# Kernel optimization log

Hardware: AMD Instinct MI355X
Metric: run time of the kernel (lower is better)

## Reference

```python
import jax, jax.numpy as jnp
import numpy as np

N = 50000   # nodes
E = 800000  # edges
H = 128     # hidden_dim
K = 4       # Chebyshev order
EPS_BN = 1e-5
EPS_L2 = 1e-12


def setup_inputs() -> dict:
    key = jax.random.key(0)
    ks = jax.random.split(key, 8)
    x = jax.random.normal(ks[0], (N, 3), dtype=jnp.float32)
    edge_index = jax.random.randint(ks[1], (2, E), 0, N, dtype=jnp.int32)

    def lin(k, fi, fo):
        s = 1.0 / np.sqrt(fi)
        return jax.random.uniform(k, (fi, fo), jnp.float32, -s, s)

    def cheb_params(k, fi, fo):
        kk = jax.random.split(k, K)
        W = jnp.stack([lin(kk[i], fi, fo) for i in range(K)])  # [K, fi, fo]
        b = jnp.zeros((fo,), jnp.float32)
        return W, b

    W1, b1 = cheb_params(ks[2], 3, H)
    W2, b2 = cheb_params(ks[3], H, H)
    W3, b3 = cheb_params(ks[4], H, H)
    W4, b4 = cheb_params(ks[5], H, H)
    Wr = lin(ks[6], H, 3)
    br = jnp.zeros((3,), jnp.float32)
    ones = jnp.ones((H,), jnp.float32)
    zeros = jnp.zeros((H,), jnp.float32)
    return {
        'x': x, 'edge_index': edge_index,
        'W1': W1, 'b1': b1, 'W2': W2, 'b2': b2,
        'W3': W3, 'b3': b3, 'W4': W4, 'b4': b4,
        'g1': ones, 'be1': zeros, 'g2': ones, 'be2': zeros,
        'g3': ones, 'be3': zeros, 'Wr': Wr, 'br': br,
    }


def _prop(h, src, dst, norm):
    # one sparse Laplacian application: out[dst] += norm * h[src]
    return jax.ops.segment_sum(norm[:, None] * h[src], dst, num_segments=N)


def _cheb(h, src, dst, norm, W, b):
    # PyG ChebConv with sym normalization, lambda_max=2 -> L_hat edge weights
    # are -D^-1/2 A D^-1/2 with zero diagonal (encoded in norm).
    out = h @ W[0]
    Tx0, Tx1 = h, _prop(h, src, dst, norm)
    out = out + Tx1 @ W[1]
    for k in range(2, W.shape[0]):
        Tx2 = 2.0 * _prop(Tx1, src, dst, norm) - Tx0
        out = out + Tx2 @ W[k]
        Tx0, Tx1 = Tx1, Tx2
    return out + b


def _bn(h, g, b):
    # BatchNorm1d in training mode: batch stats over node dim, biased var
    m = h.mean(axis=0)
    v = h.var(axis=0)
    return g * (h - m) * jax.lax.rsqrt(v + EPS_BN) + b


def reference(x, edge_index, W1, b1, W2, b2, W3, b3, W4, b4,
              g1, be1, g2, be2, g3, be3, Wr, br):
    src, dst = edge_index[0], edge_index[1]
    deg = jax.ops.segment_sum(jnp.ones((E,), jnp.float32), src, num_segments=N)
    dinv = jnp.where(deg > 0, jax.lax.rsqrt(jnp.maximum(deg, 1.0)), 0.0)
    norm = -dinv[src] * dinv[dst]

    h = _bn(jax.nn.leaky_relu(_cheb(x, src, dst, norm, W1, b1)), g1, be1)
    h = _bn(jax.nn.leaky_relu(_cheb(h, src, dst, norm, W2, b2)), g2, be2)
    h = _bn(jax.nn.relu(_cheb(h, src, dst, norm, W3, b3)), g3, be3)
    h = _cheb(h, src, dst, norm, W4, b4)
    # F.normalize(p=2, dim=1)
    h = h / jnp.maximum(jnp.linalg.norm(h, axis=1, keepdims=True), EPS_L2)
    return h @ Wr + br
```

## Files before the change

kernel.cpp:

```cpp
#include <hip/hip_runtime.h>
#include <hip/hip_fp16.h>

#define HD 128

typedef __attribute__((ext_vector_type(8))) _Float16 f16x8;
typedef __attribute__((ext_vector_type(4))) float f32x4;
typedef unsigned int u32;

struct h4s { __half2 a, b; };

__device__ __forceinline__ float lrelu(float x, float s) { return x > 0.f ? x : s * x; }

__global__ void k_edge_count(const int* __restrict__ src, const int* __restrict__ dst,
                             int* __restrict__ degc, int* __restrict__ cnt,
                             int* __restrict__ ledge, int E) {
  int e = blockIdx.x * blockDim.x + threadIdx.x;
  if (e < E) {
    atomicAdd(&degc[src[e]], 1);
    ledge[e] = atomicAdd(&cnt[dst[e]], 1);
  }
}

__global__ __launch_bounds__(1024) void k_scan1(const int* __restrict__ cnt,
                                                int* __restrict__ rowptr,
                                                int* __restrict__ bsums, int n) {
  __shared__ int buf[1024];
  int i = blockIdx.x * 1024 + threadIdx.x;
  int v = (i < n) ? cnt[i] : 0;
  buf[threadIdx.x] = v;
  __syncthreads();
  for (int o = 1; o < 1024; o <<= 1) {
    int t = (threadIdx.x >= (unsigned)o) ? buf[threadIdx.x - o] : 0;
    __syncthreads();
    buf[threadIdx.x] += t;
    __syncthreads();
  }
  if (i < n) rowptr[i] = buf[threadIdx.x] - v;
  if (threadIdx.x == 1023) bsums[blockIdx.x] = buf[1023];
}

__global__ __launch_bounds__(1024) void k_scan3(int* __restrict__ rowptr,
                                                const int* __restrict__ bsums,
                                                const int* __restrict__ degc,
                                                float* __restrict__ dinv, int n, int Etot,
                                                int nb) {
  __shared__ int blockoff;
  if (nb <= 64) {
    if (threadIdx.x < 64) {
      int lane = threadIdx.x;
      int v = (lane < nb) ? bsums[lane] : 0;
      int inc = v;
#pragma unroll
      for (int o = 1; o < 64; o <<= 1) {
        int t = __shfl_up(inc, o, 64);
        if (lane >= o) inc += t;
      }
      if (lane == (int)blockIdx.x) blockoff = inc - v;
    }
  } else if (threadIdx.x == 0) {
    int sum = 0;
    for (int t = 0; t < (int)blockIdx.x; ++t) sum += bsums[t];
    blockoff = sum;
  }
  __syncthreads();
  int i = blockIdx.x * 1024 + threadIdx.x;
  if (i < n) {
    rowptr[i] += blockoff;
    int dg = degc[i];
    dinv[i] = dg > 0 ? rsqrtf((float)dg) : 0.f;
  }
  if (i == 0) rowptr[n] = Etot;
}

__global__ void k_fill(const int* __restrict__ src, const int* __restrict__ dst,
                       const int* __restrict__ ledge, const int* __restrict__ rowptr,
                       const float* __restrict__ dinv, uint2* __restrict__ cw, int E) {
  int e = blockIdx.x * blockDim.x + threadIdx.x;
  if (e < E) {
    int s = src[e], d = dst[e];
    int p = rowptr[d] + ledge[e];
    cw[p] = make_uint2((u32)s, __float_as_uint(-dinv[s] * dinv[d]));
  }
}

__global__ void k_prop3(const int* __restrict__ rowptr, const uint2* __restrict__ cw,
                        const float* __restrict__ Hs, const float* __restrict__ Sub,
                        float* __restrict__ Out, float scale, int n) {
  int r = blockIdx.x * blockDim.x + threadIdx.x;
  if (r >= n) return;
  int b = rowptr[r], e = rowptr[r + 1];
  float a0 = 0.f, a1 = 0.f, a2 = 0.f;
  for (int j = b; j < e; ++j) {
    uint2 m = cw[j];
    int s = (int)m.x;
    float w = __uint_as_float(m.y);
    a0 = fmaf(w, Hs[s * 3 + 0], a0);
    a1 = fmaf(w, Hs[s * 3 + 1], a1);
    a2 = fmaf(w, Hs[s * 3 + 2], a2);
  }
  float r0 = scale * a0, r1 = scale * a1, r2 = scale * a2;
  if (Sub) { r0 -= Sub[r * 3 + 0]; r1 -= Sub[r * 3 + 1]; r2 -= Sub[r * 3 + 2]; }
  Out[r * 3 + 0] = r0; Out[r * 3 + 1] = r1; Out[r * 3 + 2] = r2;
}

template <int PHI>
__global__ __launch_bounds__(256) void k_prop128(
    const int* __restrict__ rowptr, const uint2* __restrict__ cw,
    const __half* __restrict__ Ph, const __half* __restrict__ Sub,
    __half* __restrict__ Outh, float scale, int n,
    const float* __restrict__ gsc, const float* __restrict__ gsh,
    const float* __restrict__ ssc, const float* __restrict__ ssh, float slope) {
  int r = blockIdx.x * 4 + (int)(threadIdx.x >> 6);
  int lane = threadIdx.x & 63;
  if (r >= n) return;
  int b = rowptr[r], e = rowptr[r + 1];
  int fl = (lane & 31) << 2;
  int half = lane >> 5;
  float ax = 0.f, ay = 0.f, az = 0.f, aw = 0.f, ws = 0.f;
  int j = b;
  for (; j + 7 < e; j += 8) {
    h4s h[4];
    float w[4];
#pragma unroll
    for (int q = 0; q < 4; ++q) {
      int idx = j + 2 * q + half;
      uint2 m = cw[idx];
      w[q] = __uint_as_float(m.y);
      h[q] = *(const h4s*)&Ph[(size_t)m.x * HD + fl];
    }
#pragma unroll
    for (int q = 0; q < 4; ++q) {
      float2 f0 = __half22float2(h[q].a);
      float2 f1 = __half22float2(h[q].b);
      if (PHI) {
        f0.x = lrelu(f0.x, slope); f0.y = lrelu(f0.y, slope);
        f1.x = lrelu(f1.x, slope); f1.y = lrelu(f1.y, slope);
        ws += w[q];
      }
      ax = fmaf(w[q], f0.x, ax);
      ay = fmaf(w[q], f0.y, ay);
      az = fmaf(w[q], f1.x, az);
      aw = fmaf(w[q], f1.y, aw);
    }
  }
  for (; j + 1 < e; j += 2) {
    int idx = j + half;
    uint2 m = cw[idx];
    float w = __uint_as_float(m.y);
    h4s h = *(const h4s*)&Ph[(size_t)m.x * HD + fl];
    float2 f0 = __half22float2(h.a);
    float2 f1 = __half22float2(h.b);
    if (PHI) {
      f0.x = lrelu(f0.x, slope); f0.y = lrelu(f0.y, slope);
      f1.x = lrelu(f1.x, slope); f1.y = lrelu(f1.y, slope);
      ws += w;
    }
    ax = fmaf(w, f0.x, ax);
    ay = fmaf(w, f0.y, ay);
    az = fmaf(w, f1.x, az);
    aw = fmaf(w, f1.y, aw);
  }
  if (j < e && half == 0) {
    uint2 m = cw[j];
    float w = __uint_as_float(m.y);
    h4s h = *(const h4s*)&Ph[(size_t)m.x * HD + fl];
    float2 f0 = __half22float2(h.a);
    float2 f1 = __half22float2(h.b);
    if (PHI) {
      f0.x = lrelu(f0.x, slope); f0.y = lrelu(f0.y, slope);
      f1.x = lrelu(f1.x, slope); f1.y = lrelu(f1.y, slope);
      ws += w;
    }
    ax = fmaf(w, f0.x, ax);
    ay = fmaf(w, f0.y, ay);
    az = fmaf(w, f1.x, az);
    aw = fmaf(w, f1.y, aw);
  }
  ax += __shfl_xor(ax, 32, 64);
  ay += __shfl_xor(ay, 32, 64);
  az += __shfl_xor(az, 32, 64);
  aw += __shfl_xor(aw, 32, 64);
  if (PHI) {
    ws += __shfl_xor(ws, 32, 64);
    float4 g4 = *(const float4*)&gsc[fl];
    float4 s4 = *(const float4*)&gsh[fl];
    ax = fmaf(ax, g4.x, ws * s4.x);
    ay = fmaf(ay, g4.y, ws * s4.y);
    az = fmaf(az, g4.z, ws * s4.z);
    aw = fmaf(aw, g4.w, ws * s4.w);
  }
  float4 o = make_float4(scale * ax, scale * ay, scale * az, scale * aw);
  if (Sub) {
    h4s sh4 = *(const h4s*)&Sub[(size_t)r * HD + fl];
    float2 s0 = __half22float2(sh4.a);
    float2 s1 = __half22float2(sh4.b);
    if (ssc != nullptr) {
      float4 c4 = *(const float4*)&ssc[fl];
      float4 d4 = *(const float4*)&ssh[fl];
      s0.x = fmaf(lrelu(s0.x, slope), c4.x, d4.x);
      s0.y = fmaf(lrelu(s0.y, slope), c4.y, d4.y);
      s1.x = fmaf(lrelu(s1.x, slope), c4.z, d4.z);
      s1.y = fmaf(lrelu(s1.y, slope), c4.w, d4.w);
    }
    o.x -= s0.x; o.y -= s0.y; o.z -= s1.x; o.w -= s1.y;
  }
  if (half == 0) {
    h4s ho;
    ho.a = __float22half2_rn(make_float2(o.x, o.y));
    ho.b = __float22half2_rn(make_float2(o.z, o.w));
    *(h4s*)&Outh[(size_t)r * HD + fl] = ho;
  }
}

__global__ __launch_bounds__(128) void k_l1gemm(
    const float* __restrict__ X, const float* __restrict__ T1, const float* __restrict__ T2,
    const float* __restrict__ T3, const float* __restrict__ W1, const float* __restrict__ b1,
    __half* __restrict__ Outh, float* __restrict__ bnsum, float* __restrict__ bnsq,
    float slope, int n, int rpb) {
  int j = threadIdx.x;
  float w[12];
#pragma unroll
  for (int t = 0; t < 4; ++t)
#pragma unroll
    for (int c = 0; c < 3; ++c) w[t * 3 + c] = W1[(t * 3 + c) * HD + j];
  float bj = b1[j];
  int r0 = blockIdx.x * rpb, r1 = min(r0 + rpb, n);
  float s = 0.f, q = 0.f;
  for (int r = r0; r < r1; ++r) {
    float acc = bj;
#pragma unroll
    for (int c = 0; c < 3; ++c) {
      acc = fmaf(X [r * 3 + c], w[0 + c], acc);
      acc = fmaf(T1[r * 3 + c], w[3 + c], acc);
      acc = fmaf(T2[r * 3 + c], w[6 + c], acc);
      acc = fmaf(T3[r * 3 + c], w[9 + c], acc);
    }
    Outh[(size_t)r * HD + j] = __float2half(acc);
    float a = lrelu(acc, slope);
    s += a;
    q = fmaf(a, a, q);
  }
  atomicAdd(&bnsum[j], s);
  atomicAdd(&bnsq[j], q);
}

__global__ void k_wsplit3(const float* __restrict__ W2, const float* __restrict__ W3,
                          const float* __restrict__ W4, uint4* __restrict__ Whi,
                          uint4* __restrict__ Wlo) {
  int flat = blockIdx.x * 256 + threadIdx.x;
  int wsel = flat >> 13;
  int f = flat & 8191;
  const float* W = (wsel == 0) ? W2 : (wsel == 1) ? W3 : W4;
  int n = f & 127, K8 = f >> 7;
  int chunk = K8 >> 2, g = K8 & 3;
  f16x8 hv, lv;
#pragma unroll
  for (int i = 0; i < 8; ++i) {
    int k = chunk * 32 + ((i >> 2) << 4) + g * 4 + (i & 3);
    float v = W[(size_t)k * HD + n];
    _Float16 hh = (_Float16)v;
    _Float16 hl = (_Float16)(v - (float)hh);
    hv[i] = hh;
    lv[i] = hl;
  }
  int slot = chunk * 512 + (n >> 4) * 64 + g * 16 + (n & 15);
  Whi[wsel * 8192 + slot] = *(uint4*)&hv;
  Wlo[wsel * 8192 + slot] = *(uint4*)&lv;
}

__global__ __launch_bounds__(256) void k_gemm4m(
    const __half* __restrict__ T0, const __half* __restrict__ T1,
    const __half* __restrict__ T2, const __half* __restrict__ T3,
    const uint4* __restrict__ Whi, const uint4* __restrict__ Wlo,
    const float* __restrict__ bias, __half* __restrict__ OUTh,
    float* bnsum, float* bnsq, float stat_slope,
    const float* __restrict__ gsc, const float* __restrict__ gsh, float phi_slope,
    int nrows) {
  __shared__ __half sA[2048];
  __shared__ __half sWh[4096], sWl[4096];
  __shared__ float redS[128], redQ[128];

  int tid = threadIdx.x;
  int lane = tid & 63, w = tid >> 6, wr = w >> 1, wc = w & 1;
  int g = (tid >> 4) & 3;
  int ri = tid & 15;
  int row0 = blockIdx.x * 64;
  int arow = row0 + w * 16 + ri;
  bool aval = arow < nrows;

  f32x4 zero = {0.f, 0.f, 0.f, 0.f};
  f32x4 acc[2][4];
#pragma unroll
  for (int mi = 0; mi < 2; ++mi)
#pragma unroll
    for (int nj = 0; nj < 4; ++nj) acc[mi][nj] = zero;

  if (tid < 128) { redS[tid] = 0.f; redQ[tid] = 0.f; }

  for (int chunk = 0; chunk < 16; ++chunk) {
    const __half* Ts = (chunk < 4) ? T0 : (chunk < 8) ? T1 : (chunk < 12) ? T2 : T3;
    int kc = chunk & 3;
    h4s va, vb;
    *(uint2*)&va = make_uint2(0u, 0u);
    *(uint2*)&vb = make_uint2(0u, 0u);
    if (aval) {
      const __half* ap = Ts + (size_t)arow * HD + kc * 32 + g * 4;
      va = *(const h4s*)ap;
      vb = *(const h4s*)(ap + 16);
    }
    size_t wbase = (size_t)chunk * 512;
    uint4 wh0 = Whi[wbase + tid], wh1 = Whi[wbase + 256 + tid];
    uint4 wl0 = Wlo[wbase + tid], wl1 = Wlo[wbase + 256 + tid];

    __syncthreads();

    if (gsc != nullptr && chunk < 4) {
      float fv[8];
      float2 f0 = __half22float2(va.a), f1 = __half22float2(va.b);
      float2 f2 = __half22float2(vb.a), f3 = __half22float2(vb.b);
      fv[0] = f0.x; fv[1] = f0.y; fv[2] = f1.x; fv[3] = f1.y;
      fv[4] = f2.x; fv[5] = f2.y; fv[6] = f3.x; fv[7] = f3.y;
#pragma unroll
      for (int i = 0; i < 8; ++i) {
        int f = kc * 32 + g * 4 + (i & 3) + ((i >> 2) << 4);
        fv[i] = fmaf(lrelu(fv[i], phi_slope), gsc[f], gsh[f]);
      }
      va.a = __float22half2_rn(make_float2(fv[0], fv[1]));
      va.b = __float22half2_rn(make_float2(fv[2], fv[3]));
      vb.a = __float22half2_rn(make_float2(fv[4], fv[5]));
      vb.b = __float22half2_rn(make_float2(fv[6], fv[7]));
    }
    *(h4s*)&sA[tid * 8] = va;
    *(h4s*)&sA[tid * 8 + 4] = vb;
    *(uint4*)&sWh[tid * 8] = wh0;
    *(uint4*)&sWh[(256 + tid) * 8] = wh1;
    *(uint4*)&sWl[tid * 8] = wl0;
    *(uint4*)&sWl[(256 + tid) * 8] = wl1;
    __syncthreads();

    f16x8 a[2], bh[4], bl[4];
#pragma unroll
    for (int mi = 0; mi < 2; ++mi)
      a[mi] = *(const f16x8*)&sA[((wr * 2 + mi) * 64 + lane) * 8];
#pragma unroll
    for (int nj = 0; nj < 4; ++nj) {
      bh[nj] = *(const f16x8*)&sWh[((wc * 4 + nj) * 64 + lane) * 8];
      bl[nj] = *(const f16x8*)&sWl[((wc * 4 + nj) * 64 + lane) * 8];
    }
#pragma unroll
    for (int mi = 0; mi < 2; ++mi)
#pragma unroll
      for (int nj = 0; nj < 4; ++nj) {
        acc[mi][nj] = __builtin_amdgcn_mfma_f32_16x16x32_f16(a[mi], bh[nj], acc[mi][nj], 0, 0, 0);
        acc[mi][nj] = __builtin_amdgcn_mfma_f32_16x16x32_f16(a[mi], bl[nj], acc[mi][nj], 0, 0, 0);
      }
  }

  int l4 = (lane >> 4) * 4, ni = lane & 15;
  bool stats = (bnsum != nullptr);
#pragma unroll
  for (int nj = 0; nj < 4; ++nj) {
    int c = wc * 64 + nj * 16 + ni;
    float bcol = bias[c];
    float s = 0.f, q = 0.f;
#pragma unroll
    for (int mi = 0; mi < 2; ++mi)
#pragma unroll
      for (int j = 0; j < 4; ++j) {
        int row = row0 + (wr * 2 + mi) * 16 + l4 + j;
        if (row < nrows) {
          float v = acc[mi][nj][j] + bcol;
          OUTh[(size_t)row * HD + c] = __float2half(v);
          if (stats) {
            float a = lrelu(v, stat_slope);
            s += a;
            q = fmaf(a, a, q);
          }
        }
      }
    if (stats) {
      s += __shfl_xor(s, 16, 64);
      s += __shfl_xor(s, 32, 64);
      q += __shfl_xor(q, 16, 64);
      q += __shfl_xor(q, 32, 64);
      if (lane < 16) {
        atomicAdd(&redS[c], s);
        atomicAdd(&redQ[c], q);
      }
    }
  }
  if (stats) {
    __syncthreads();
    if (tid < 128) {
      atomicAdd(&bnsum[tid], redS[tid]);
      atomicAdd(&bnsq[tid], redQ[tid]);
    }
  }
}

__global__ void k_bnfin(const float* __restrict__ bsum, const float* __restrict__ bsq,
                        const float* __restrict__ g, const float* __restrict__ be,
                        float* __restrict__ scaleb, float* __restrict__ shiftb, int n) {
  int f = threadIdx.x;
  if (f < HD) {
    float m = bsum[f] / (float)n;
    float v = bsq[f] / (float)n - m * m;
    float rs = rsqrtf(v + 1e-5f);
    float sc = g[f] * rs;
    scaleb[f] = sc;
    shiftb[f] = be[f] - m * sc;
  }
}

__global__ __launch_bounds__(256) void k_final(const __half* __restrict__ Hb,
                                               const float* __restrict__ Wr,
                                               const float* __restrict__ br,
                                               float* __restrict__ out, int n) {
  int r = blockIdx.x * 4 + (int)(threadIdx.x >> 6);
  int lane = threadIdx.x & 63;
  if (r >= n) return;
  float h0 = __half2float(Hb[(size_t)r * HD + lane]);
  float h1 = __half2float(Hb[(size_t)r * HD + 64 + lane]);
  float ss = h0 * h0 + h1 * h1;
#pragma unroll
  for (int o = 32; o; o >>= 1) ss += __shfl_xor(ss, o, 64);
  float inv = 1.f / fmaxf(sqrtf(ss), 1e-12f);
  h0 *= inv; h1 *= inv;
  float o0 = h0 * Wr[lane * 3 + 0] + h1 * Wr[(64 + lane) * 3 + 0];
  float o1 = h0 * Wr[lane * 3 + 1] + h1 * Wr[(64 + lane) * 3 + 1];
  float o2 = h0 * Wr[lane * 3 + 2] + h1 * Wr[(64 + lane) * 3 + 2];
#pragma unroll
  for (int o = 32; o; o >>= 1) {
    o0 += __shfl_xor(o0, o, 64);
    o1 += __shfl_xor(o1, o, 64);
    o2 += __shfl_xor(o2, o, 64);
  }
  if (lane == 0) {
    out[r * 3 + 0] = o0 + br[0];
    out[r * 3 + 1] = o1 + br[1];
    out[r * 3 + 2] = o2 + br[2];
  }
}

extern "C" void kernel_launch(void* const* d_in, const int* in_sizes, int n_in,
                              void* d_out, int out_size, void* d_ws, size_t ws_size,
                              hipStream_t stream) {
  const float* x  = (const float*)d_in[0];
  const int*   ei = (const int*)d_in[1];
  const float* W1 = (const float*)d_in[2];
  const float* b1 = (const float*)d_in[3];
  const float* W2 = (const float*)d_in[4];
  const float* b2 = (const float*)d_in[5];
  const float* W3 = (const float*)d_in[6];
  const float* b3 = (const float*)d_in[7];
  const float* W4 = (const float*)d_in[8];
  const float* b4 = (const float*)d_in[9];
  const float* g1 = (const float*)d_in[10];
  const float* be1= (const float*)d_in[11];
  const float* g2 = (const float*)d_in[12];
  const float* be2= (const float*)d_in[13];
  const float* g3 = (const float*)d_in[14];
  const float* be3= (const float*)d_in[15];
  const float* Wr = (const float*)d_in[16];
  const float* br = (const float*)d_in[17];

  const int N = in_sizes[0] / 3;
  const int E = in_sizes[1] / 2;
  const int* src = ei;
  const int* dst = ei + E;
  float* out = (float*)d_out;

  char* wp = (char*)d_ws;
  size_t used = 0;
  auto alloc = [&](size_t bytes) -> void* {
    void* p = (void*)(wp + used);
    used += (bytes + 255) & ~(size_t)255;
    return p;
  };
  int*   deg2   = (int*)alloc((size_t)2 * N * 4);
  int*   rowptr = (int*)alloc((size_t)(N + 1) * 4);
  float* dinv   = (float*)alloc((size_t)N * 4);
  int*   bsums  = (int*)alloc(256 * 4);
  int*   ledge  = (int*)alloc((size_t)E * 4);
  uint2* cw     = (uint2*)alloc((size_t)E * 8);
  float* t1     = (float*)alloc((size_t)N * 3 * 4);
  float* t2     = (float*)alloc((size_t)N * 3 * 4);
  float* t3     = (float*)alloc((size_t)N * 3 * 4);
  __half* phA   = (__half*)alloc((size_t)N * HD * 2);
  __half* phB   = (__half*)alloc((size_t)N * HD * 2);
  __half* phC   = (__half*)alloc((size_t)N * HD * 2);
  __half* phD   = (__half*)alloc((size_t)N * HD * 2);
  float* stats  = (float*)alloc(6 * HD * 4);
  float* scsh   = (float*)alloc(6 * HD * 4);
  uint4* Whi3   = (uint4*)alloc(3 * 8192 * 16);
  uint4* Wlo3   = (uint4*)alloc(3 * 8192 * 16);
  if (used > ws_size) return;

  int* degc = deg2;
  int* cnt  = deg2 + N;
  float* bnsum1 = stats + 0 * HD; float* bnsq1 = stats + 1 * HD;
  float* bnsum2 = stats + 2 * HD; float* bnsq2 = stats + 3 * HD;
  float* bnsum3 = stats + 4 * HD; float* bnsq3 = stats + 5 * HD;
  float* sc1 = scsh + 0 * HD; float* sh1 = scsh + 1 * HD;
  float* sc2 = scsh + 2 * HD; float* sh2 = scsh + 3 * HD;
  float* sc3 = scsh + 4 * HD; float* sh3 = scsh + 5 * HD;

  const int eb = (E + 255) / 256;
  const int nb = (N + 255) / 256;
  const int pb = (N + 3) / 4;
  const int sb = (N + 1023) / 1024;
  const int gbm = (N + 63) / 64;

  hipMemsetAsync(stats, 0, 6 * HD * 4, stream);
  hipMemsetAsync(deg2, 0, (size_t)2 * N * 4, stream);
  k_edge_count<<<eb, 256, 0, stream>>>(src, dst, degc, cnt, ledge, E);
  k_scan1<<<sb, 1024, 0, stream>>>(cnt, rowptr, bsums, N);
  k_scan3<<<sb, 1024, 0, stream>>>(rowptr, bsums, degc, dinv, N, E, sb);
  k_fill<<<eb, 256, 0, stream>>>(src, dst, ledge, rowptr, dinv, cw, E);
  k_wsplit3<<<96, 256, 0, stream>>>(W2, W3, W4, Whi3, Wlo3);

  k_prop3<<<nb, 256, 0, stream>>>(rowptr, cw, x, nullptr, t1, 1.f, N);
  k_prop3<<<nb, 256, 0, stream>>>(rowptr, cw, t1, x, t2, 2.f, N);
  k_prop3<<<nb, 256, 0, stream>>>(rowptr, cw, t2, t1, t3, 2.f, N);
  k_l1gemm<<<(N + 255) / 256, 128, 0, stream>>>(x, t1, t2, t3, W1, b1, phA,
                                                bnsum1, bnsq1, 0.01f, N, 256);
  k_bnfin<<<1, 128, 0, stream>>>(bnsum1, bnsq1, g1, be1, sc1, sh1, N);

  auto cheb_layer = [&](const uint4* Whi, const uint4* Wlo, const float* bk,
                        const float* psc, const float* psh, float phi_slope,
                        float* bs, float* bq, float stat_slope) {
    k_prop128<1><<<pb, 256, 0, stream>>>(rowptr, cw, phA, nullptr, phB, 1.f, N,
                                         psc, psh, nullptr, nullptr, phi_slope);
    k_prop128<0><<<pb, 256, 0, stream>>>(rowptr, cw, phB, phA, phC, 2.f, N,
                                         nullptr, nullptr, psc, psh, phi_slope);
    k_prop128<0><<<pb, 256, 0, stream>>>(rowptr, cw, phC, phB, phD, 2.f, N,
                                         nullptr, nullptr, nullptr, nullptr, 0.f);
    k_gemm4m<<<gbm, 256, 0, stream>>>(phA, phB, phC, phD, Whi, Wlo, bk, phA,
                                      bs, bq, stat_slope, psc, psh, phi_slope, N);
  };

  cheb_layer(Whi3, Wlo3, b2, sc1, sh1, 0.01f, bnsum2, bnsq2, 0.01f);
  k_bnfin<<<1, 128, 0, stream>>>(bnsum2, bnsq2, g2, be2, sc2, sh2, N);
  cheb_layer(Whi3 + 8192, Wlo3 + 8192, b3, sc2, sh2, 0.01f, bnsum3, bnsq3, 0.0f);
  k_bnfin<<<1, 128, 0, stream>>>(bnsum3, bnsq3, g3, be3, sc3, sh3, N);
  cheb_layer(Whi3 + 16384, Wlo3 + 16384, b4, sc3, sh3, 0.0f, nullptr, nullptr, 0.0f);

  k_final<<<pb, 256, 0, stream>>>(phA, Wr, br, out, N);
}
```

Measured before the change: 677.1 us.

## Fuse BN finalize into consumers and final normalize+projection into last GEMM

```diff
diff --git a/kernel.cpp b/kernel.cpp
--- a/kernel.cpp
+++ b/kernel.cpp
@@ -10,6 +10,14 @@
 struct h4s { __half2 a, b; };
 
 __device__ __forceinline__ float lrelu(float x, float s) { return x > 0.f ? x : s * x; }
+
+__device__ __forceinline__ float2 bn_coeff(const float* st, const float* g,
+                                           const float* be, float invn, int f) {
+  float m = st[f] * invn;
+  float v = st[HD + f] * invn - m * m;
+  float sc = g[f] * rsqrtf(v + 1e-5f);
+  return make_float2(sc, be[f] - m * sc);
+}
 
 __global__ void k_edge_count(const int* __restrict__ src, const int* __restrict__ dst,
                              int* __restrict__ degc, int* __restrict__ cnt,
@@ -23,7 +31,9 @@
 
 __global__ __launch_bounds__(1024) void k_scan1(const int* __restrict__ cnt,
                                                 int* __restrict__ rowptr,
-                                                int* __restrict__ bsums, int n) {
+                                                int* __restrict__ bsums,
+                                                float* __restrict__ stats, int n) {
+  if (blockIdx.x == 0 && threadIdx.x < 6 * HD) stats[threadIdx.x] = 0.f;
   __shared__ int buf[1024];
   int i = blockIdx.x * 1024 + threadIdx.x;
   int v = (i < n) ? cnt[i] : 0;
@@ -107,9 +117,10 @@
 __global__ __launch_bounds__(256) void k_prop128(
     const int* __restrict__ rowptr, const uint2* __restrict__ cw,
     const __half* __restrict__ Ph, const __half* __restrict__ Sub,
-    __half* __restrict__ Outh, float scale, int n,
-    const float* __restrict__ gsc, const float* __restrict__ gsh,
-    const float* __restrict__ ssc, const float* __restrict__ ssh, float slope) {
+    __half* __restrict__ Outh, float scale, int n, float invn,
+    const float* __restrict__ gst, const float* __restrict__ gg, const float* __restrict__ gbe,
+    const float* __restrict__ sst, const float* __restrict__ sg, const float* __restrict__ sbe,
+    float slope) {
   int r = blockIdx.x * 4 + (int)(threadIdx.x >> 6);
   int lane = threadIdx.x & 63;
   if (r >= n) return;
@@ -182,25 +193,29 @@
   aw += __shfl_xor(aw, 32, 64);
   if (PHI) {
     ws += __shfl_xor(ws, 32, 64);
-    float4 g4 = *(const float4*)&gsc[fl];
-    float4 s4 = *(const float4*)&gsh[fl];
-    ax = fmaf(ax, g4.x, ws * s4.x);
-    ay = fmaf(ay, g4.y, ws * s4.y);
-    az = fmaf(az, g4.z, ws * s4.z);
-    aw = fmaf(aw, g4.w, ws * s4.w);
+    float2 c0 = bn_coeff(gst, gg, gbe, invn, fl + 0);
+    float2 c1 = bn_coeff(gst, gg, gbe, invn, fl + 1);
+    float2 c2 = bn_coeff(gst, gg, gbe, invn, fl + 2);
+    float2 c3 = bn_coeff(gst, gg, gbe, invn, fl + 3);
+    ax = fmaf(ax, c0.x, ws * c0.y);
+    ay = fmaf(ay, c1.x, ws * c1.y);
+    az = fmaf(az, c2.x, ws * c2.y);
+    aw = fmaf(aw, c3.x, ws * c3.y);
   }
   float4 o = make_float4(scale * ax, scale * ay, scale * az, scale * aw);
   if (Sub) {
     h4s sh4 = *(const h4s*)&Sub[(size_t)r * HD + fl];
     float2 s0 = __half22float2(sh4.a);
     float2 s1 = __half22float2(sh4.b);
-    if (ssc != nullptr) {
-      float4 c4 = *(const float4*)&ssc[fl];
-      float4 d4 = *(const float4*)&ssh[fl];
-      s0.x = fmaf(lrelu(s0.x, slope), c4.x, d4.x);
-      s0.y = fmaf(lrelu(s0.y, slope), c4.y, d4.y);
-      s1.x = fmaf(lrelu(s1.x, slope), c4.z, d4.z);
-      s1.y = fmaf(lrelu(s1.y, slope), c4.w, d4.w);
+    if (sst != nullptr) {
+      float2 d0 = bn_coeff(sst, sg, sbe, invn, fl + 0);
+      float2 d1 = bn_coeff(sst, sg, sbe, invn, fl + 1);
+      float2 d2 = bn_coeff(sst, sg, sbe, invn, fl + 2);
+      float2 d3 = bn_coeff(sst, sg, sbe, invn, fl + 3);
+      s0.x = fmaf(lrelu(s0.x, slope), d0.x, d0.y);
+      s0.y = fmaf(lrelu(s0.y, slope), d1.x, d1.y);
+      s1.x = fmaf(lrelu(s1.x, slope), d2.x, d2.y);
+      s1.y = fmaf(lrelu(s1.y, slope), d3.x, d3.y);
     }
     o.x -= s0.x; o.y -= s0.y; o.z -= s1.x; o.w -= s1.y;
   }
@@ -274,11 +289,15 @@
     const uint4* __restrict__ Whi, const uint4* __restrict__ Wlo,
     const float* __restrict__ bias, __half* __restrict__ OUTh,
     float* bnsum, float* bnsq, float stat_slope,
-    const float* __restrict__ gsc, const float* __restrict__ gsh, float phi_slope,
+    const float* __restrict__ gst, const float* __restrict__ gg,
+    const float* __restrict__ gbe, float invn, float phi_slope,
+    const float* __restrict__ Wr, const float* __restrict__ br, float* __restrict__ outp,
     int nrows) {
   __shared__ __half sA[2048];
   __shared__ __half sWh[4096], sWl[4096];
   __shared__ float redS[128], redQ[128];
+  __shared__ float fss[64];
+  __shared__ float fob[64][3];
 
   int tid = threadIdx.x;
   int lane = tid & 63, w = tid >> 6, wr = w >> 1, wc = w & 1;
@@ -296,6 +315,7 @@
     for (int nj = 0; nj < 4; ++nj) acc[mi][nj] = zero;
 
   if (tid < 128) { redS[tid] = 0.f; redQ[tid] = 0.f; }
+  if (tid < 64) { fss[tid] = 0.f; fob[tid][0] = 0.f; fob[tid][1] = 0.f; fob[tid][2] = 0.f; }
 
   for (int chunk = 0; chunk < 16; ++chunk) {
     const __half* Ts = (chunk < 4) ? T0 : (chunk < 8) ? T1 : (chunk < 12) ? T2 : T3;
@@ -314,7 +334,7 @@
 
     __syncthreads();
 
-    if (gsc != nullptr && chunk < 4) {
+    if (gst != nullptr && chunk < 4) {
       float fv[8];
       float2 f0 = __half22float2(va.a), f1 = __half22float2(va.b);
       float2 f2 = __half22float2(vb.a), f3 = __half22float2(vb.b);
@@ -323,7 +343,8 @@
 #pragma unroll
       for (int i = 0; i < 8; ++i) {
         int f = kc * 32 + g * 4 + (i & 3) + ((i >> 2) << 4);
-        fv[i] = fmaf(lrelu(fv[i], phi_slope), gsc[f], gsh[f]);
+        float2 cs = bn_coeff(gst, gg, gbe, invn, f);
+        fv[i] = fmaf(lrelu(fv[i], phi_slope), cs.x, cs.y);
       }
       va.a = __float22half2_rn(make_float2(fv[0], fv[1]));
       va.b = __float22half2_rn(make_float2(fv[2], fv[3]));
@@ -357,88 +378,118 @@
   }
 
   int l4 = (lane >> 4) * 4, ni = lane & 15;
-  bool stats = (bnsum != nullptr);
-#pragma unroll
-  for (int nj = 0; nj < 4; ++nj) {
-    int c = wc * 64 + nj * 16 + ni;
-    float bcol = bias[c];
-    float s = 0.f, q = 0.f;
-#pragma unroll
-    for (int mi = 0; mi < 2; ++mi)
-#pragma unroll
-      for (int j = 0; j < 4; ++j) {
-        int row = row0 + (wr * 2 + mi) * 16 + l4 + j;
-        if (row < nrows) {
-          float v = acc[mi][nj][j] + bcol;
-          OUTh[(size_t)row * HD + c] = __float2half(v);
-          if (stats) {
-            float a = lrelu(v, stat_slope);
-            s += a;
-            q = fmaf(a, a, q);
+
+  if (outp == nullptr) {
+    bool stats = (bnsum != nullptr);
+#pragma unroll
+    for (int nj = 0; nj < 4; ++nj) {
+      int c = wc * 64 + nj * 16 + ni;
+      float bcol = bias[c];
+      float s = 0.f, q = 0.f;
+#pragma unroll
+      for (int mi = 0; mi < 2; ++mi)
+#pragma unroll
+        for (int j = 0; j < 4; ++j) {
+          int row = row0 + (wr * 2 + mi) * 16 + l4 + j;
+          if (row < nrows) {
+            float v = acc[mi][nj][j] + bcol;
+            OUTh[(size_t)row * HD + c] = __float2half(v);
+            if (stats) {
+              float a = lrelu(v, stat_slope);
+              s += a;
+              q = fmaf(a, a, q);
+            }
           }
         }
-      }
+      if (stats) {
+        s += __shfl_xor(s, 16, 64);
+        s += __shfl_xor(s, 32, 64);
+        q += __shfl_xor(q, 16, 64);
+        q += __shfl_xor(q, 32, 64);
+        if (lane < 16) {
+          atomicAdd(&redS[c], s);
+          atomicAdd(&redQ[c], q);
+        }
+      }
+    }
     if (stats) {
-      s += __shfl_xor(s, 16, 64);
-      s += __shfl_xor(s, 32, 64);
-      q += __shfl_xor(q, 16, 64);
-      q += __shfl_xor(q, 32, 64);
-      if (lane < 16) {
-        atomicAdd(&redS[c], s);
-        atomicAdd(&redQ[c], q);
-      }
-    }
-  }
-  if (stats) {
-    __syncthreads();
-    if (tid < 128) {
-      atomicAdd(&bnsum[tid], redS[tid]);
-      atomicAdd(&bnsq[tid], redQ[tid]);
-    }
-  }
-}
-
-__global__ void k_bnfin(const float* __restrict__ bsum, const float* __restrict__ bsq,
-                        const float* __restrict__ g, const float* __restrict__ be,
-                        float* __restrict__ scaleb, float* __restrict__ shiftb, int n) {
-  int f = threadIdx.x;
-  if (f < HD) {
-    float m = bsum[f] / (float)n;
-    float v = bsq[f] / (float)n - m * m;
-    float rs = rsqrtf(v + 1e-5f);
-    float sc = g[f] * rs;
-    scaleb[f] = sc;
-    shiftb[f] = be[f] - m * sc;
-  }
-}
-
-__global__ __launch_bounds__(256) void k_final(const __half* __restrict__ Hb,
-                                               const float* __restrict__ Wr,
-                                               const float* __restrict__ br,
-                                               float* __restrict__ out, int n) {
-  int r = blockIdx.x * 4 + (int)(threadIdx.x >> 6);
-  int lane = threadIdx.x & 63;
-  if (r >= n) return;
-  float h0 = __half2float(Hb[(size_t)r * HD + lane]);
-  float h1 = __half2float(Hb[(size_t)r * HD + 64 + lane]);
-  float ss = h0 * h0 + h1 * h1;
-#pragma unroll
-  for (int o = 32; o; o >>= 1) ss += __shfl_xor(ss, o, 64);
-  float inv = 1.f / fmaxf(sqrtf(ss), 1e-12f);
-  h0 *= inv; h1 *= inv;
-  float o0 = h0 * Wr[lane * 3 + 0] + h1 * Wr[(64 + lane) * 3 + 0];
-  float o1 = h0 * Wr[lane * 3 + 1] + h1 * Wr[(64 + lane) * 3 + 1];
-  float o2 = h0 * Wr[lane * 3 + 2] + h1 * Wr[(64 + lane) * 3 + 2];
-#pragma unroll
-  for (int o = 32; o; o >>= 1) {
-    o0 += __shfl_xor(o0, o, 64);
-    o1 += __shfl_xor(o1, o, 64);
-    o2 += __shfl_xor(o2, o, 64);
-  }
-  if (lane == 0) {
-    out[r * 3 + 0] = o0 + br[0];
-    out[r * 3 + 1] = o1 + br[1];
-    out[r * 3 + 2] = o2 + br[2];
+      __syncthreads();
+      if (tid < 128) {
+        atomicAdd(&bnsum[tid], redS[tid]);
+        atomicAdd(&bnsq[tid], redQ[tid]);
+      }
+    }
+  } else {
+    __syncthreads();
+    float ss8[2][4];
+#pragma unroll
+    for (int mi = 0; mi < 2; ++mi)
+#pragma unroll
+      for (int j = 0; j < 4; ++j) ss8[mi][j] = 0.f;
+#pragma unroll
+    for (int nj = 0; nj < 4; ++nj) {
+      int c = wc * 64 + nj * 16 + ni;
+      float bcol = bias[c];
+#pragma unroll
+      for (int mi = 0; mi < 2; ++mi)
+#pragma unroll
+        for (int j = 0; j < 4; ++j) {
+          float v = acc[mi][nj][j] + bcol;
+          ss8[mi][j] = fmaf(v, v, ss8[mi][j]);
+        }
+    }
+#pragma unroll
+    for (int mk = 1; mk <= 8; mk <<= 1)
+#pragma unroll
+      for (int mi = 0; mi < 2; ++mi)
+#pragma unroll
+        for (int j = 0; j < 4; ++j) ss8[mi][j] += __shfl_xor(ss8[mi][j], mk, 64);
+    if (ni == 0) {
+#pragma unroll
+      for (int mi = 0; mi < 2; ++mi)
+#pragma unroll
+        for (int j = 0; j < 4; ++j)
+          atomicAdd(&fss[(wr * 2 + mi) * 16 + l4 + j], ss8[mi][j]);
+    }
+    __syncthreads();
+    if (tid < 64) fss[tid] = 1.f / fmaxf(sqrtf(fss[tid]), 1e-12f);
+    __syncthreads();
+#pragma unroll
+    for (int mi = 0; mi < 2; ++mi)
+#pragma unroll
+      for (int j = 0; j < 4; ++j) {
+        int rl = (wr * 2 + mi) * 16 + l4 + j;
+        float inv = fss[rl];
+        float o0 = 0.f, o1 = 0.f, o2 = 0.f;
+#pragma unroll
+        for (int nj = 0; nj < 4; ++nj) {
+          int c = wc * 64 + nj * 16 + ni;
+          float v = (acc[mi][nj][j] + bias[c]) * inv;
+          o0 = fmaf(v, Wr[c * 3 + 0], o0);
+          o1 = fmaf(v, Wr[c * 3 + 1], o1);
+          o2 = fmaf(v, Wr[c * 3 + 2], o2);
+        }
+#pragma unroll
+        for (int mk = 1; mk <= 8; mk <<= 1) {
+          o0 += __shfl_xor(o0, mk, 64);
+          o1 += __shfl_xor(o1, mk, 64);
+          o2 += __shfl_xor(o2, mk, 64);
+        }
+        if (ni == 0) {
+          atomicAdd(&fob[rl][0], o0);
+          atomicAdd(&fob[rl][1], o1);
+          atomicAdd(&fob[rl][2], o2);
+        }
+      }
+    __syncthreads();
+    if (tid < 64) {
+      int row = row0 + tid;
+      if (row < nrows) {
+        outp[row * 3 + 0] = fob[tid][0] + br[0];
+        outp[row * 3 + 1] = fob[tid][1] + br[1];
+        outp[row * 3 + 2] = fob[tid][2] + br[2];
+      }
+    }
   }
 }
 
@@ -469,6 +520,7 @@
   const int* src = ei;
   const int* dst = ei + E;
   float* out = (float*)d_out;
+  const float invn = 1.0f / (float)N;
 
   char* wp = (char*)d_ws;
   size_t used = 0;
@@ -491,19 +543,15 @@
   __half* phC   = (__half*)alloc((size_t)N * HD * 2);
   __half* phD   = (__half*)alloc((size_t)N * HD * 2);
   float* stats  = (float*)alloc(6 * HD * 4);
-  float* scsh   = (float*)alloc(6 * HD * 4);
   uint4* Whi3   = (uint4*)alloc(3 * 8192 * 16);
   uint4* Wlo3   = (uint4*)alloc(3 * 8192 * 16);
   if (used > ws_size) return;
 
   int* degc = deg2;
   int* cnt  = deg2 + N;
-  float* bnsum1 = stats + 0 * HD; float* bnsq1 = stats + 1 * HD;
-  float* bnsum2 = stats + 2 * HD; float* bnsq2 = stats + 3 * HD;
-  float* bnsum3 = stats + 4 * HD; float* bnsq3 = stats + 5 * HD;
-  float* sc1 = scsh + 0 * HD; float* sh1 = scsh + 1 * HD;
-  float* sc2 = scsh + 2 * HD; float* sh2 = scsh + 3 * HD;
-  float* sc3 = scsh + 4 * HD; float* sh3 = scsh + 5 * HD;
+  float* st1 = stats + 0 * HD;
+  float* st2 = stats + 2 * HD;
+  float* st3 = stats + 4 * HD;
 
   const int eb = (E + 255) / 256;
   const int nb = (N + 255) / 256;
@@ -511,10 +559,9 @@
   const int sb = (N + 1023) / 1024;
   const int gbm = (N + 63) / 64;
 
-  hipMemsetAsync(stats, 0, 6 * HD * 4, stream);
   hipMemsetAsync(deg2, 0, (size_t)2 * N * 4, stream);
   k_edge_count<<<eb, 256, 0, stream>>>(src, dst, degc, cnt, ledge, E);
-  k_scan1<<<sb, 1024, 0, stream>>>(cnt, rowptr, bsums, N);
+  k_scan1<<<sb, 1024, 0, stream>>>(cnt, rowptr, bsums, stats, N);
   k_scan3<<<sb, 1024, 0, stream>>>(rowptr, bsums, degc, dinv, N, E, sb);
   k_fill<<<eb, 256, 0, stream>>>(src, dst, ledge, rowptr, dinv, cw, E);
   k_wsplit3<<<96, 256, 0, stream>>>(W2, W3, W4, Whi3, Wlo3);
@@ -523,27 +570,27 @@
   k_prop3<<<nb, 256, 0, stream>>>(rowptr, cw, t1, x, t2, 2.f, N);
   k_prop3<<<nb, 256, 0, stream>>>(rowptr, cw, t2, t1, t3, 2.f, N);
   k_l1gemm<<<(N + 255) / 256, 128, 0, stream>>>(x, t1, t2, t3, W1, b1, phA,
-                                                bnsum1, bnsq1, 0.01f, N, 256);
-  k_bnfin<<<1, 128, 0, stream>>>(bnsum1, bnsq1, g1, be1, sc1, sh1, N);
+                                                st1, st1 + HD, 0.01f, N, 256);
 
   auto cheb_layer = [&](const uint4* Whi, const uint4* Wlo, const float* bk,
-                        const float* psc, const float* psh, float phi_slope,
-                        float* bs, float* bq, float stat_slope) {
-    k_prop128<1><<<pb, 256, 0, stream>>>(rowptr, cw, phA, nullptr, phB, 1.f, N,
-                                         psc, psh, nullptr, nullptr, phi_slope);
-    k_prop128<0><<<pb, 256, 0, stream>>>(rowptr, cw, phB, phA, phC, 2.f, N,
-                                         nullptr, nullptr, psc, psh, phi_slope);
-    k_prop128<0><<<pb, 256, 0, stream>>>(rowptr, cw, phC, phB, phD, 2.f, N,
-                                         nullptr, nullptr, nullptr, nullptr, 0.f);
+                        const float* gst, const float* gg, const float* gbe, float phi_slope,
+                        float* so, float stat_slope,
+                        const float* Wrp, const float* brp, float* outp) {
+    k_prop128<1><<<pb, 256, 0, stream>>>(rowptr, cw, phA, nullptr, phB, 1.f, N, invn,
+                                         gst, gg, gbe, nullptr, nullptr, nullptr, phi_slope);
+    k_prop128<0><<<pb, 256, 0, stream>>>(rowptr, cw, phB, phA, phC, 2.f, N, invn,
+                                         nullptr, nullptr, nullptr, gst, gg, gbe, phi_slope);
+    k_prop128<0><<<pb, 256, 0, stream>>>(rowptr, cw, phC, phB, phD, 2.f, N, invn,
+                                         nullptr, nullptr, nullptr, nullptr, nullptr, nullptr,
+                                         0.f);
     k_gemm4m<<<gbm, 256, 0, stream>>>(phA, phB, phC, phD, Whi, Wlo, bk, phA,
-                                      bs, bq, stat_slope, psc, psh, phi_slope, N);
+                                      so, so ? so + HD : nullptr, stat_slope,
+                                      gst, gg, gbe, invn, phi_slope,
+                                      Wrp, brp, outp, N);
   };
 
-  cheb_layer(Whi3, Wlo3, b2, sc1, sh1, 0.01f, bnsum2, bnsq2, 0.01f);
-  k_bnfin<<<1, 128, 0, stream>>>(bnsum2, bnsq2, g2, be2, sc2, sh2, N);
-  cheb_layer(Whi3 + 8192, Wlo3 + 8192, b3, sc2, sh2, 0.01f, bnsum3, bnsq3, 0.0f);
-  k_bnfin<<<1, 128, 0, stream>>>(bnsum3, bnsq3, g3, be3, sc3, sh3, N);
-  cheb_layer(Whi3 + 16384, Wlo3 + 16384, b4, sc3, sh3, 0.0f, nullptr, nullptr, 0.0f);
-
-  k_final<<<pb, 256, 0, stream>>>(phA, Wr, br, out, N);
-}
+  cheb_layer(Whi3, Wlo3, b2, st1, g1, be1, 0.01f, st2, 0.01f, nullptr, nullptr, nullptr);
+  cheb_layer(Whi3 + 8192, Wlo3 + 8192, b3, st2, g2, be2, 0.01f, st3, 0.0f,
+             nullptr, nullptr, nullptr);
+  cheb_layer(Whi3 + 16384, Wlo3 + 16384, b4, st3, g3, be3, 0.0f, nullptr, 0.0f, Wr, br, out);
+}
```

Result: no change. 672.2 us (median of 2 runs) (-0.7%).
